# Kernel optimization log

Hardware: AMD Instinct MI355X
Metric: run time of the kernel (lower is better)

Reference implementation:

```python
import jax, jax.numpy as jnp
import numpy as np

N_NODES = 50000
N_EDGES = 800000
IN_DIM = 64
H_DIM = 64


def setup_inputs() -> dict:
    key = jax.random.key(0)
    ks = jax.random.split(key, 6)
    feat = jax.random.normal(ks[0], (N_NODES, IN_DIM), dtype=jnp.float32)
    W1 = jax.random.normal(ks[1], (IN_DIM, H_DIM), dtype=jnp.float32) * (1.0 / np.sqrt(IN_DIM))
    b1 = jnp.zeros((H_DIM,), dtype=jnp.float32)
    W2 = jax.random.normal(ks[2], (H_DIM, 1), dtype=jnp.float32) * (1.0 / np.sqrt(H_DIM))
    b2 = jnp.zeros((1,), dtype=jnp.float32)
    src = jax.random.randint(ks[3], (N_EDGES,), 0, N_NODES, dtype=jnp.int32)
    dst = jax.random.randint(ks[4], (N_EDGES,), 0, N_NODES, dtype=jnp.int32)
    return {"feat": feat, "W1": W1, "b1": b1, "W2": W2, "b2": b2, "src": src, "dst": dst}


def _norms(src, dst, n_nodes):
    # DGL GraphConv norm='both': symmetric D^{-1/2} A D^{-1/2}, degrees clamped to >=1
    ones = jnp.ones(src.shape[0], dtype=jnp.float32)
    out_deg = jax.ops.segment_sum(ones, src, num_segments=n_nodes)
    in_deg = jax.ops.segment_sum(ones, dst, num_segments=n_nodes)
    out_norm = jax.lax.rsqrt(jnp.clip(out_deg, 1.0))
    in_norm = jax.lax.rsqrt(jnp.clip(in_deg, 1.0))
    return out_norm, in_norm


def _graph_conv(feat, W, b, src, dst, out_norm, in_norm, act):
    h = feat * out_norm[:, None]          # scale source features by D_out^{-1/2}
    msg = h[src]                          # gather along edges [E, d]
    agg = jax.ops.segment_sum(msg, dst, num_segments=feat.shape[0])  # scatter-sum to dst
    agg = agg * in_norm[:, None]          # scale by D_in^{-1/2}
    return act(agg @ W + b)


def reference(feat, W1, b1, W2, b2, src, dst):
    out_norm, in_norm = _norms(src, dst, feat.shape[0])
    h = _graph_conv(feat, W1, b1, src, dst, out_norm, in_norm, jax.nn.relu)
    return _graph_conv(h, W2, b2, src, dst, out_norm, in_norm, jax.nn.sigmoid)
```

## Files before the change

### kernel.cpp

```cpp
#include <hip/hip_runtime.h>
#include <hip/hip_fp16.h>
#include <math.h>


#define BS 256
#define EPB 2048
#define SCB 2048

__global__ __launch_bounds__(256, 4)
void histA_featw1_kernel(const int* __restrict__ src, const int* __restrict__ dst,
                         const float* __restrict__ feat, const float* __restrict__ W1,
                         int* __restrict__ dhist, int* __restrict__ out_deg,
                         __half* __restrict__ featp,
                         int E, int N, int NB, int T) {
    __shared__ float4 ftile[64 * 16];
    __shared__ int histD[256];
    int tid = threadIdx.x;
    if ((int)blockIdx.x < T) {
        histD[tid] = 0;
        __syncthreads();
        int base = blockIdx.x * EPB;
        #pragma unroll
        for (int it = 0; it < EPB / BS; it++) {
            int e = base + it * BS + tid;
            if (e < E) {
                atomicAdd(&histD[dst[e] >> 8], 1);
                atomicAdd(&out_deg[src[e]], 1);
            }
        }
        __syncthreads();
        if (tid < NB) dhist[tid * T + (int)blockIdx.x] = histD[tid];
    } else {
        int lane = tid & 63;
        int wave = tid >> 6;
        #define WD(i) float wv##i = W1[(i) * 64 + lane];
        WD(0)  WD(1)  WD(2)  WD(3)  WD(4)  WD(5)  WD(6)  WD(7)
        WD(8)  WD(9)  WD(10) WD(11) WD(12) WD(13) WD(14) WD(15)
        WD(16) WD(17) WD(18) WD(19) WD(20) WD(21) WD(22) WD(23)
        WD(24) WD(25) WD(26) WD(27) WD(28) WD(29) WD(30) WD(31)
        WD(32) WD(33) WD(34) WD(35) WD(36) WD(37) WD(38) WD(39)
        WD(40) WD(41) WD(42) WD(43) WD(44) WD(45) WD(46) WD(47)
        WD(48) WD(49) WD(50) WD(51) WD(52) WD(53) WD(54) WD(55)
        WD(56) WD(57) WD(58) WD(59) WD(60) WD(61) WD(62) WD(63)
        #undef WD
        int rBase = ((int)blockIdx.x - T) * 64;
        const float4* feat4 = (const float4*)feat;
        int maxF4 = N * 16 - 1;
        #pragma unroll
        for (int it = 0; it < 4; it++) {
            int idx = it * BS + tid;
            ftile[idx] = feat4[min(rBase * 16 + idx, maxF4)];
        }
        __syncthreads();
        #pragma unroll 1
        for (int rr = 0; rr < 16; rr++) {
            int r = wave * 16 + rr;
            const float4* ft = &ftile[r * 16];
            float a0 = 0.0f, a1 = 0.0f, a2 = 0.0f, a3 = 0.0f;
            #define RK(k4, wA, wB, wC, wD_) { float4 f = ft[k4]; \
                a0 = fmaf(f.x, wA, a0); a1 = fmaf(f.y, wB, a1); \
                a2 = fmaf(f.z, wC, a2); a3 = fmaf(f.w, wD_, a3); }
            RK(0,  wv0,  wv1,  wv2,  wv3)  RK(1,  wv4,  wv5,  wv6,  wv7)
            RK(2,  wv8,  wv9,  wv10, wv11) RK(3,  wv12, wv13, wv14, wv15)
            RK(4,  wv16, wv17, wv18, wv19) RK(5,  wv20, wv21, wv22, wv23)
            RK(6,  wv24, wv25, wv26, wv27) RK(7,  wv28, wv29, wv30, wv31)
            RK(8,  wv32, wv33, wv34, wv35) RK(9,  wv36, wv37, wv38, wv39)
            RK(10, wv40, wv41, wv42, wv43) RK(11, wv44, wv45, wv46, wv47)
            RK(12, wv48, wv49, wv50, wv51) RK(13, wv52, wv53, wv54, wv55)
            RK(14, wv56, wv57, wv58, wv59) RK(15, wv60, wv61, wv62, wv63)
            #undef RK
            int rowg = rBase + r;
            if (rowg < N)
                featp[(size_t)rowg * 64 + lane] = __float2half((a0 + a1) + (a2 + a3));
        }
    }
}

__global__ void scan1_kernel(const int* __restrict__ dhist, int* __restrict__ bsum, int M) {
    __shared__ int s[256];
    int t = threadIdx.x;
    int base = blockIdx.x * SCB + t * 8;
    int sum = 0;
    #pragma unroll
    for (int i = 0; i < 8; i++) {
        int k = base + i;
        if (k < M) sum += dhist[k];
    }
    s[t] = sum; __syncthreads();
    for (int off = 1; off < 256; off <<= 1) {
        int u = (t >= off) ? s[t - off] : 0; __syncthreads();
        s[t] += u; __syncthreads();
    }
    if (t == 255) bsum[blockIdx.x] = s[255];
}

__global__ void scan2_kernel(int* __restrict__ bsum, int NSB) {
    __shared__ int s[256];
    int t = threadIdx.x;
    int v = (t < NSB) ? bsum[t] : 0;
    s[t] = v; __syncthreads();
    for (int off = 1; off < 256; off <<= 1) {
        int u = (t >= off) ? s[t - off] : 0; __syncthreads();
        s[t] += u; __syncthreads();
    }
    if (t < NSB) bsum[t] = s[t] - v;
}

__global__ void scan3_kernel(int* __restrict__ dhist, const int* __restrict__ bsum, int M) {
    __shared__ int s[256];
    int t = threadIdx.x;
    int base = blockIdx.x * SCB + t * 8;
    int v[8];
    int sum = 0;
    #pragma unroll
    for (int i = 0; i < 8; i++) {
        int k = base + i;
        v[i] = (k < M) ? dhist[k] : 0;
        sum += v[i];
    }
    s[t] = sum; __syncthreads();
    for (int off = 1; off < 256; off <<= 1) {
        int u = (t >= off) ? s[t - off] : 0; __syncthreads();
        s[t] += u; __syncthreads();
    }
    int run = bsum[blockIdx.x] + s[t] - sum;
    #pragma unroll
    for (int i = 0; i < 8; i++) {
        int k = base + i;
        if (k < M) dhist[k] = run;
        run += v[i];
    }
}

__global__ void partition_kernel(const int* __restrict__ src, const int* __restrict__ dst,
                                 const int* __restrict__ dhist,
                                 int* __restrict__ packed, int E, int NB, int T) {
    __shared__ int arr[256];
    int tid = threadIdx.x;
    int b = blockIdx.x;
    arr[tid] = (tid < NB) ? dhist[tid * T + b] : 0;
    __syncthreads();
    int base = b * EPB;
    #pragma unroll
    for (int it = 0; it < EPB / BS; it++) {
        int e = base + it * BS + tid;
        if (e < E) {
            int d = dst[e], s2 = src[e];
            int pos = atomicAdd(&arr[d >> 8], 1);
            packed[pos] = s2 | ((d & 255) << 17);
        }
    }
}

__global__ void finalize_kernel(const int* __restrict__ dhist,
                                const int* __restrict__ packed,
                                int* __restrict__ csr_src, int* __restrict__ in_deg,
                                int* __restrict__ row_start, const int* __restrict__ out_deg,
                                __half* __restrict__ featp,
                                int N, int NB, int T, int E) {
    __shared__ int hist[256];
    __shared__ int sc[256];
    int tid = threadIdx.x;
    int b = blockIdx.x;
    int lo = dhist[b * T];
    int hi = (b + 1 < NB) ? dhist[(b + 1) * T] : E;
    hist[tid] = 0; __syncthreads();
    for (int i = lo + tid; i < hi; i += BS)
        atomicAdd(&hist[(packed[i] >> 17) & 255], 1);
    __syncthreads();
    int v = hist[tid];
    sc[tid] = v; __syncthreads();
    for (int off = 1; off < 256; off <<= 1) {
        int u = (tid >= off) ? sc[tid - off] : 0; __syncthreads();
        sc[tid] += u; __syncthreads();
    }
    int ex = sc[tid] - v;
    int n = b * 256 + tid;
    if (n < N) { in_deg[n] = v; row_start[n] = lo + ex; }
    sc[tid] = lo + ex;
    __syncthreads();
    for (int i = lo + tid; i < hi; i += BS) {
        int pv = packed[i];
        int pos = atomicAdd(&sc[(pv >> 17) & 255], 1);
        csr_src[pos] = pv & 0x1FFFF;
    }
    __syncthreads();
    float* snorm = (float*)sc;
    snorm[tid] = rsqrtf(fmaxf((float)((n < N) ? out_deg[n] : 1), 1.0f));
    __syncthreads();
    int nodes = min(256, N - b * 256);
    uint4* fp = (uint4*)(featp + (size_t)b * 256 * 64);
    int total = nodes * 8;
    for (int i = tid; i < total; i += BS) {
        float s = snorm[i >> 3];
        uint4 u = fp[i];
        __half2* hh = (__half2*)&u;
        #pragma unroll
        for (int c = 0; c < 4; c++) {
            float2 p = __half22float2(hh[c]);
            p.x *= s; p.y *= s;
            hh[c] = __float22half2_rn(p);
        }
        fp[i] = u;
    }
}

__global__ void csr_agg1_kernel(const int* __restrict__ row_start, const int* __restrict__ in_deg,
                                const int* __restrict__ csr_src, const int* __restrict__ out_deg,
                                const __half* __restrict__ featp,
                                const float* __restrict__ b1, const float* __restrict__ W2,
                                float* __restrict__ s_buf, int N) {
    int gid = blockIdx.x * blockDim.x + threadIdx.x;
    int n = gid >> 6;
    if (n >= N) return;
    int lane = threadIdx.x & 63;
    int g = lane >> 3;
    int l = lane & 7;
    int start = row_start[n];
    int deg = in_deg[n];
    float acc[8] = {0, 0, 0, 0, 0, 0, 0, 0};
    const uint4* fp4 = (const uint4*)featp;
    for (int j = 0; j < deg; j += 16) {
        int e0 = j + g;
        int e1 = j + 8 + g;
        bool p0 = e0 < deg;
        bool p1 = e1 < deg;
        int sn0 = p0 ? csr_src[start + e0] : 0;
        int sn1 = p1 ? csr_src[start + e1] : 0;
        uint4 q0 = {0, 0, 0, 0}, q1 = {0, 0, 0, 0};
        if (p0) q0 = fp4[(size_t)sn0 * 8 + l];
        if (p1) q1 = fp4[(size_t)sn1 * 8 + l];
        const __half2* h0 = (const __half2*)&q0;
        const __half2* h1 = (const __half2*)&q1;
        #pragma unroll
        for (int c = 0; c < 4; c++) {
            float2 f0 = __half22float2(h0[c]);
            float2 f1 = __half22float2(h1[c]);
            acc[2 * c]     += f0.x + f1.x;
            acc[2 * c + 1] += f0.y + f1.y;
        }
    }
    #pragma unroll
    for (int off = 8; off < 64; off <<= 1) {
        #pragma unroll
        for (int c = 0; c < 8; c++)
            acc[c] += __shfl_xor(acc[c], off, 64);
    }
    float inn = rsqrtf(fmaxf((float)deg, 1.0f));
    float v = 0.0f;
    #pragma unroll
    for (int c = 0; c < 8; c++) {
        float h = fmaxf(inn * acc[c] + b1[l * 8 + c], 0.0f);
        v += h * W2[l * 8 + c];
    }
    #pragma unroll
    for (int off = 1; off < 8; off <<= 1)
        v += __shfl_xor(v, off, 64);
    if (lane == 0)
        s_buf[n] = rsqrtf(fmaxf((float)out_deg[n], 1.0f)) * v;
}

__global__ void csr_agg2_kernel(const int* __restrict__ row_start, const int* __restrict__ in_deg,
                                const int* __restrict__ csr_src,
                                const float* __restrict__ s_buf, const float* __restrict__ b2,
                                float* __restrict__ out, int N) {
    int gid = blockIdx.x * blockDim.x + threadIdx.x;
    int n = gid >> 4;
    if (n >= N) return;
    int sub = gid & 15;
    int start = row_start[n];
    int deg = in_deg[n];
    float a = 0.0f;
    for (int j = sub; j < deg; j += 32) {
        int j1 = j + 16;
        int i0 = csr_src[start + j];
        int i1 = (j1 < deg) ? csr_src[start + j1] : 0;
        float v0 = s_buf[i0];
        float v1 = (j1 < deg) ? s_buf[i1] : 0.0f;
        a += v0 + v1;
    }
    #pragma unroll
    for (int off = 1; off < 16; off <<= 1)
        a += __shfl_xor(a, off, 64);
    if (sub == 0) {
        float x = rsqrtf(fmaxf((float)deg, 1.0f)) * a + b2[0];
        out[n] = 1.0f / (1.0f + expf(-x));
    }
}

extern "C" void kernel_launch(void* const* d_in, const int* in_sizes, int n_in,
                              void* d_out, int out_size, void* d_ws, size_t ws_size,
                              hipStream_t stream) {
    const float* feat = (const float*)d_in[0];
    const float* W1   = (const float*)d_in[1];
    const float* b1   = (const float*)d_in[2];
    const float* W2   = (const float*)d_in[3];
    const float* b2   = (const float*)d_in[4];
    const int* src = (const int*)d_in[5];
    const int* dst = (const int*)d_in[6];
    float* out = (float*)d_out;

    const int N  = in_sizes[0] / 64;
    const int E  = in_sizes[5];
    const int NB = (N + 255) >> 8;
    const int T  = (E + EPB - 1) / EPB;
    const int M  = NB * T;
    const int NSB = (M + SCB - 1) / SCB;

    int* wsi = (int*)d_ws;
    int* bsum        = wsi;
    int* in_deg      = bsum + NSB;
    int* row_start   = in_deg + N;
    int* out_deg     = row_start + N;
    int* dhist       = out_deg + N;
    int* packed      = dhist + M;
    int* csr_src     = packed + E;
    size_t int_bytes = ((size_t)NSB + 3 * (size_t)N + (size_t)M + 2 * (size_t)E) * sizeof(int);
    size_t half_off  = (int_bytes + 15) & ~(size_t)15;
    __half* featp = (__half*)((char*)d_ws + half_off);
    float* s_buf  = (float*)((char*)d_ws + half_off + (size_t)64 * N * sizeof(__half));

    hipMemsetAsync(out_deg, 0, (size_t)N * sizeof(int), stream);

    histA_featw1_kernel<<<T + (N + 63) / 64, BS, 0, stream>>>(
        src, dst, feat, W1, dhist, out_deg, featp, E, N, NB, T);
    scan1_kernel<<<NSB, 256, 0, stream>>>(dhist, bsum, M);
    scan2_kernel<<<1, 256, 0, stream>>>(bsum, NSB);
    scan3_kernel<<<NSB, 256, 0, stream>>>(dhist, bsum, M);
    partition_kernel<<<T, BS, 0, stream>>>(src, dst, dhist, packed, E, NB, T);
    finalize_kernel<<<NB, BS, 0, stream>>>(
        dhist, packed, csr_src, in_deg, row_start, out_deg, featp, N, NB, T, E);
    csr_agg1_kernel<<<(int)(((size_t)N * 64 + BS - 1) / BS), BS, 0, stream>>>(
        row_start, in_deg, csr_src, out_deg, featp, b1, W2, s_buf, N);
    csr_agg2_kernel<<<(int)(((size_t)N * 16 + BS - 1) / BS), BS, 0, stream>>>(
        row_start, in_deg, csr_src, s_buf, b2, out, N);
}
```

Baseline: 183.0 us.

## Replace global out-degree atomics with bucketed source partition counting

Out-degree counting switches from per-edge global atomics into out_deg to a per-block shared-memory histogram over source buckets. The bucket counts are scanned together with the destination histogram, and each edge's low source byte is scattered into a byte array partitioned by source bucket. Finalize launches extra blocks that count out-degrees per bucket in shared memory and then apply the feature normalization. This removes the memset and the contended global atomics, at the cost of a second partition write, a doubled scan and more finalize blocks.

New measurement: 158.5 us (median of 2 runs). 13.4% less time.

```diff
diff --git a/kernel.cpp b/kernel.cpp
--- a/kernel.cpp
+++ b/kernel.cpp
@@ -10,14 +10,15 @@
 __global__ __launch_bounds__(256, 4)
 void histA_featw1_kernel(const int* __restrict__ src, const int* __restrict__ dst,
                          const float* __restrict__ feat, const float* __restrict__ W1,
-                         int* __restrict__ dhist, int* __restrict__ out_deg,
+                         int* __restrict__ dhist,
                          __half* __restrict__ featp,
-                         int E, int N, int NB, int T) {
+                         int E, int N, int NB, int T, int M) {
     __shared__ float4 ftile[64 * 16];
     __shared__ int histD[256];
+    __shared__ int histS[256];
     int tid = threadIdx.x;
     if ((int)blockIdx.x < T) {
-        histD[tid] = 0;
+        histD[tid] = 0; histS[tid] = 0;
         __syncthreads();
         int base = blockIdx.x * EPB;
         #pragma unroll
@@ -25,11 +26,14 @@
             int e = base + it * BS + tid;
             if (e < E) {
                 atomicAdd(&histD[dst[e] >> 8], 1);
-                atomicAdd(&out_deg[src[e]], 1);
+                atomicAdd(&histS[src[e] >> 8], 1);
             }
         }
         __syncthreads();
-        if (tid < NB) dhist[tid * T + (int)blockIdx.x] = histD[tid];
+        if (tid < NB) {
+            dhist[tid * T + (int)blockIdx.x] = histD[tid];
+            dhist[M + tid * T + (int)blockIdx.x] = histS[tid];
+        }
     } else {
         int lane = tid & 63;
         int wave = tid >> 6;
@@ -76,7 +80,7 @@
     }
 }
 
-__global__ void scan1_kernel(const int* __restrict__ dhist, int* __restrict__ bsum, int M) {
+__global__ void scan1_kernel(const int* __restrict__ dhist, int* __restrict__ bsum, int M2) {
     __shared__ int s[256];
     int t = threadIdx.x;
     int base = blockIdx.x * SCB + t * 8;
@@ -84,7 +88,7 @@
     #pragma unroll
     for (int i = 0; i < 8; i++) {
         int k = base + i;
-        if (k < M) sum += dhist[k];
+        if (k < M2) sum += dhist[k];
     }
     s[t] = sum; __syncthreads();
     for (int off = 1; off < 256; off <<= 1) {
@@ -106,7 +110,7 @@
     if (t < NSB) bsum[t] = s[t] - v;
 }
 
-__global__ void scan3_kernel(int* __restrict__ dhist, const int* __restrict__ bsum, int M) {
+__global__ void scan3_kernel(int* __restrict__ dhist, const int* __restrict__ bsum, int M2) {
     __shared__ int s[256];
     int t = threadIdx.x;
     int base = blockIdx.x * SCB + t * 8;
@@ -115,7 +119,7 @@
     #pragma unroll
     for (int i = 0; i < 8; i++) {
         int k = base + i;
-        v[i] = (k < M) ? dhist[k] : 0;
+        v[i] = (k < M2) ? dhist[k] : 0;
         sum += v[i];
     }
     s[t] = sum; __syncthreads();
@@ -127,18 +131,21 @@
     #pragma unroll
     for (int i = 0; i < 8; i++) {
         int k = base + i;
-        if (k < M) dhist[k] = run;
+        if (k < M2) dhist[k] = run;
         run += v[i];
     }
 }
 
 __global__ void partition_kernel(const int* __restrict__ src, const int* __restrict__ dst,
                                  const int* __restrict__ dhist,
-                                 int* __restrict__ packed, int E, int NB, int T) {
-    __shared__ int arr[256];
+                                 int* __restrict__ packed, unsigned char* __restrict__ srcPartB,
+                                 int E, int NB, int T, int M) {
+    __shared__ int darr[256];
+    __shared__ int sarr[256];
     int tid = threadIdx.x;
     int b = blockIdx.x;
-    arr[tid] = (tid < NB) ? dhist[tid * T + b] : 0;
+    darr[tid] = (tid < NB) ? dhist[tid * T + b] : 0;
+    sarr[tid] = (tid < NB) ? (dhist[M + tid * T + b] - E) : 0;
     __syncthreads();
     int base = b * EPB;
     #pragma unroll
@@ -146,62 +153,77 @@
         int e = base + it * BS + tid;
         if (e < E) {
             int d = dst[e], s2 = src[e];
-            int pos = atomicAdd(&arr[d >> 8], 1);
+            int pos = atomicAdd(&darr[d >> 8], 1);
             packed[pos] = s2 | ((d & 255) << 17);
+            int pos2 = atomicAdd(&sarr[s2 >> 8], 1);
+            srcPartB[pos2] = (unsigned char)(s2 & 255);
         }
     }
 }
 
 __global__ void finalize_kernel(const int* __restrict__ dhist,
                                 const int* __restrict__ packed,
+                                const unsigned char* __restrict__ srcPartB,
                                 int* __restrict__ csr_src, int* __restrict__ in_deg,
-                                int* __restrict__ row_start, const int* __restrict__ out_deg,
+                                int* __restrict__ row_start, int* __restrict__ out_deg,
                                 __half* __restrict__ featp,
-                                int N, int NB, int T, int E) {
+                                int N, int NB, int T, int M, int E) {
     __shared__ int hist[256];
     __shared__ int sc[256];
     int tid = threadIdx.x;
     int b = blockIdx.x;
-    int lo = dhist[b * T];
-    int hi = (b + 1 < NB) ? dhist[(b + 1) * T] : E;
-    hist[tid] = 0; __syncthreads();
-    for (int i = lo + tid; i < hi; i += BS)
-        atomicAdd(&hist[(packed[i] >> 17) & 255], 1);
-    __syncthreads();
-    int v = hist[tid];
-    sc[tid] = v; __syncthreads();
-    for (int off = 1; off < 256; off <<= 1) {
-        int u = (tid >= off) ? sc[tid - off] : 0; __syncthreads();
-        sc[tid] += u; __syncthreads();
-    }
-    int ex = sc[tid] - v;
-    int n = b * 256 + tid;
-    if (n < N) { in_deg[n] = v; row_start[n] = lo + ex; }
-    sc[tid] = lo + ex;
-    __syncthreads();
-    for (int i = lo + tid; i < hi; i += BS) {
-        int pv = packed[i];
-        int pos = atomicAdd(&sc[(pv >> 17) & 255], 1);
-        csr_src[pos] = pv & 0x1FFFF;
-    }
-    __syncthreads();
-    float* snorm = (float*)sc;
-    snorm[tid] = rsqrtf(fmaxf((float)((n < N) ? out_deg[n] : 1), 1.0f));
-    __syncthreads();
-    int nodes = min(256, N - b * 256);
-    uint4* fp = (uint4*)(featp + (size_t)b * 256 * 64);
-    int total = nodes * 8;
-    for (int i = tid; i < total; i += BS) {
-        float s = snorm[i >> 3];
-        uint4 u = fp[i];
-        __half2* hh = (__half2*)&u;
-        #pragma unroll
-        for (int c = 0; c < 4; c++) {
-            float2 p = __half22float2(hh[c]);
-            p.x *= s; p.y *= s;
-            hh[c] = __float22half2_rn(p);
-        }
-        fp[i] = u;
+    if (b < NB) {
+        int lo = dhist[b * T];
+        int hi = (b + 1 < NB) ? dhist[(b + 1) * T] : E;
+        hist[tid] = 0; __syncthreads();
+        for (int i = lo + tid; i < hi; i += BS)
+            atomicAdd(&hist[(packed[i] >> 17) & 255], 1);
+        __syncthreads();
+        int v = hist[tid];
+        sc[tid] = v; __syncthreads();
+        for (int off = 1; off < 256; off <<= 1) {
+            int u = (tid >= off) ? sc[tid - off] : 0; __syncthreads();
+            sc[tid] += u; __syncthreads();
+        }
+        int ex = sc[tid] - v;
+        int n = b * 256 + tid;
+        if (n < N) { in_deg[n] = v; row_start[n] = lo + ex; }
+        sc[tid] = lo + ex;
+        __syncthreads();
+        for (int i = lo + tid; i < hi; i += BS) {
+            int pv = packed[i];
+            int pos = atomicAdd(&sc[(pv >> 17) & 255], 1);
+            csr_src[pos] = pv & 0x1FFFF;
+        }
+    } else {
+        int sb = b - NB;
+        int lo = dhist[M + sb * T] - E;
+        int hi = ((sb + 1 < NB) ? dhist[M + (sb + 1) * T] : 2 * E) - E;
+        hist[tid] = 0; __syncthreads();
+        for (int i = lo + tid; i < hi; i += BS)
+            atomicAdd(&hist[srcPartB[i]], 1);
+        __syncthreads();
+        int n = sb * 256 + tid;
+        int od = hist[tid];
+        if (n < N) out_deg[n] = od;
+        float* snorm = (float*)sc;
+        snorm[tid] = rsqrtf(fmaxf((float)od, 1.0f));
+        __syncthreads();
+        int nodes = min(256, N - sb * 256);
+        uint4* fp = (uint4*)(featp + (size_t)sb * 256 * 64);
+        int total = nodes * 8;
+        for (int i = tid; i < total; i += BS) {
+            float s = snorm[i >> 3];
+            uint4 u = fp[i];
+            __half2* hh = (__half2*)&u;
+            #pragma unroll
+            for (int c = 0; c < 4; c++) {
+                float2 p = __half22float2(hh[c]);
+                p.x *= s; p.y *= s;
+                hh[c] = __float22half2_rn(p);
+            }
+            fp[i] = u;
+        }
     }
 }
 
@@ -305,7 +327,8 @@
     const int NB = (N + 255) >> 8;
     const int T  = (E + EPB - 1) / EPB;
     const int M  = NB * T;
-    const int NSB = (M + SCB - 1) / SCB;
+    const int M2 = 2 * M;
+    const int NSB = (M2 + SCB - 1) / SCB;
 
     int* wsi = (int*)d_ws;
     int* bsum        = wsi;
@@ -313,23 +336,23 @@
     int* row_start   = in_deg + N;
     int* out_deg     = row_start + N;
     int* dhist       = out_deg + N;
-    int* packed      = dhist + M;
+    int* packed      = dhist + M2;
     int* csr_src     = packed + E;
-    size_t int_bytes = ((size_t)NSB + 3 * (size_t)N + (size_t)M + 2 * (size_t)E) * sizeof(int);
+    unsigned char* srcPartB = (unsigned char*)(csr_src + E);
+    size_t int_bytes = ((size_t)NSB + 3 * (size_t)N + (size_t)M2 + 2 * (size_t)E) * sizeof(int)
+                     + (size_t)E;
     size_t half_off  = (int_bytes + 15) & ~(size_t)15;
     __half* featp = (__half*)((char*)d_ws + half_off);
     float* s_buf  = (float*)((char*)d_ws + half_off + (size_t)64 * N * sizeof(__half));
 
-    hipMemsetAsync(out_deg, 0, (size_t)N * sizeof(int), stream);
-
     histA_featw1_kernel<<<T + (N + 63) / 64, BS, 0, stream>>>(
-        src, dst, feat, W1, dhist, out_deg, featp, E, N, NB, T);
-    scan1_kernel<<<NSB, 256, 0, stream>>>(dhist, bsum, M);
+        src, dst, feat, W1, dhist, featp, E, N, NB, T, M);
+    scan1_kernel<<<NSB, 256, 0, stream>>>(dhist, bsum, M2);
     scan2_kernel<<<1, 256, 0, stream>>>(bsum, NSB);
-    scan3_kernel<<<NSB, 256, 0, stream>>>(dhist, bsum, M);
-    partition_kernel<<<T, BS, 0, stream>>>(src, dst, dhist, packed, E, NB, T);
-    finalize_kernel<<<NB, BS, 0, stream>>>(
-        dhist, packed, csr_src, in_deg, row_start, out_deg, featp, N, NB, T, E);
+    scan3_kernel<<<NSB, 256, 0, stream>>>(dhist, bsum, M2);
+    partition_kernel<<<T, BS, 0, stream>>>(src, dst, dhist, packed, srcPartB, E, NB, T, M);
+    finalize_kernel<<<2 * NB, BS, 0, stream>>>(
+        dhist, packed, srcPartB, csr_src, in_deg, row_start, out_deg, featp, N, NB, T, M, E);
     csr_agg1_kernel<<<(int)(((size_t)N * 64 + BS - 1) / BS), BS, 0, stream>>>(
         row_start, in_deg, csr_src, out_deg, featp, b1, W2, s_buf, N);
     csr_agg2_kernel<<<(int)(((size_t)N * 16 + BS - 1) / BS), BS, 0, stream>>>(
```
